# Kernel optimization log

Measured on AMD Instinct MI355X. Metric: run time of the kernel, lower is better.

## Reference

```python
import jax, jax.numpy as jnp
import numpy as np
from jax import lax

SOS_IDX = 1
EOS_IDX = 2

B, T, K = 32, 256, 128


def setup_inputs() -> dict:
    key = jax.random.key(0)
    k1, k2, k3, k4 = jax.random.split(key, 4)
    h = jax.random.normal(k1, (B, T, K), dtype=jnp.float32)
    transition = jax.random.normal(k2, (K, K), dtype=jnp.float32) * 0.1
    y = jax.random.randint(k3, (B, T), 0, K)
    lengths = jnp.maximum(jax.random.randint(k4, (B,), 1, T + 1), 1)
    mask = jnp.arange(T)[None, :] < lengths[:, None]  # [B, T] bool, contiguous prefix
    return {"h": h, "transition": transition, "y": y, "lengths": lengths, "mask": mask}


def reference(h, transition, y, lengths, mask):
    """CRF negative log-likelihood, same math as CRF.nll."""
    b, t_len, k = h.shape
    # crf_scores[b,t,i,j] = h[b,t,j] + transition[i,j]
    scores = h[:, :, None, :] + transition[None, None, :, :]  # [B,T,K,K]

    # Golden path score: score of transition prev_tag -> tag at each valid step.
    prev_y = jnp.concatenate(
        [jnp.full((b, 1), SOS_IDX, dtype=y.dtype), y[:, :-1]], axis=1
    )  # [B,T]
    gold = jnp.take_along_axis(
        jnp.take_along_axis(scores, prev_y[:, :, None, None], axis=2)[:, :, 0, :],
        y[:, :, None],
        axis=2,
    )[:, :, 0]  # [B,T]
    golden_scores = jnp.sum(jnp.where(mask, gold, jnp.zeros((), h.dtype)))

    # Forward (alpha) recurrence in log space; freeze alpha past sequence end.
    alpha0 = scores[:, 0, SOS_IDX, :]  # [B,K] (all lengths >= 1)
    scores_tbkk = jnp.swapaxes(scores, 0, 1)  # [T,B,K,K]
    mask_tb = jnp.swapaxes(mask, 0, 1)  # [T,B]

    def step(alpha, xs):
        s_t, m_t = xs  # [B,K,K], [B]
        new_alpha = jax.nn.logsumexp(s_t + alpha[:, :, None], axis=1)  # [B,K]
        return jnp.where(m_t[:, None], new_alpha, alpha), None

    alpha, _ = lax.scan(step, alpha0, (scores_tbkk[1:], mask_tb[1:]))
    Z = jnp.sum(alpha[:, EOS_IDX])
    loss = (Z - golden_scores) / b
    return loss
```

## Files before the change

### kernel.cpp

```cpp
#include <hip/hip_runtime.h>
#include <stdint.h>

#define SOS_IDX 1
#define EOS_IDX 2
#define Bb 32
#define Tt 256
#define Kk 128
#define SK 136

typedef unsigned short ushort_t;
typedef __attribute__((ext_vector_type(8))) short short8;
typedef __attribute__((ext_vector_type(4))) float float4v;

__device__ __forceinline__ ushort_t f2bf(float x) {
    union { float f; uint32_t u; } c; c.f = x;
    uint32_t u = c.u + 0x7FFFu + ((c.u >> 16) & 1u);
    return (ushort_t)(u >> 16);
}
__device__ __forceinline__ float bf2f(ushort_t s) {
    union { uint32_t u; float f; } c; c.u = ((uint32_t)s) << 16;
    return c.f;
}
__device__ __forceinline__ float bflo(uint32_t u) {
    union { uint32_t u; float f; } c; c.u = u << 16; return c.f;
}
__device__ __forceinline__ float bfhi(uint32_t u) {
    union { uint32_t u; float f; } c; c.u = u & 0xFFFF0000u; return c.f;
}
__device__ __forceinline__ uint32_t pk2bf(float a, float b) {
    union { float f; uint32_t u; } ca, cb; ca.f = a; cb.f = b;
    uint32_t ua = ca.u + 0x7FFFu + ((ca.u >> 16) & 1u);
    uint32_t ub = cb.u + 0x7FFFu + ((cb.u >> 16) & 1u);
    return __builtin_amdgcn_perm(ub, ua, 0x07060302u);
}

__global__ __launch_bounds__(256, 2) void crf_stageA(const float* __restrict__ h,
                                                     const float* __restrict__ trans,
                                                     const int* __restrict__ lengths,
                                                     ushort_t* __restrict__ Qt,
                                                     float* __restrict__ Ls,
                                                     int NC, int CSPAN) {
    const int st = blockIdx.x, c = blockIdx.y, b = blockIdx.z;
    const int tid = threadIdx.x;
    const int lane = tid & 63, w = tid >> 6;
    const int c15 = lane & 15, q = lane >> 4;
    const int len = lengths[b];
    int ts = c * CSPAN; if (ts < 1) ts = 1;
    int te = (c + 1) * CSPAN; if (te > Tt) te = Tt;
    const int tE = te < len ? te : len;
    const size_t qoff = ((size_t)b * NC + c) * (Kk * Kk);
    const int nbase = st * 32;

    if (ts >= tE) {
#pragma unroll
        for (int j = 0; j < 2; ++j) {
            int idx = j * 256 + tid;
            int n = idx & 127, o = idx >> 7;
            uint4 gv; ushort_t* gp = (ushort_t*)&gv;
#pragma unroll
            for (int r = 0; r < 8; ++r) gp[r] = (n == nbase + o * 8 + r) ? (ushort_t)0x3F80 : (ushort_t)0;
            *(uint4*)&Qt[qoff + (size_t)n * Kk + nbase + o * 8] = gv;
        }
        if (tid == 0) Ls[(((size_t)b * NC + c) << 2) + st] = 0.0f;
        return;
    }

    __shared__ __align__(16) ushort_t s_S[2][32 * SK];
    __shared__ float s_wmax[2][4];

    short8 afr[2][4];
#pragma unroll
    for (int round = 0; round < 2; ++round) {
        for (int i = 0; i < 32; ++i) {
            int item = i * 256 + tid;
            int m = item & 63, k = item >> 6;
            s_S[m >> 5][(m & 31) * SK + k] = f2bf(__expf(trans[k * Kk + round * 64 + m]));
        }
        __syncthreads();
        if ((w >> 1) == round) {
            const ushort_t* sb = s_S[w & 1];
#pragma unroll
            for (int mt = 0; mt < 2; ++mt)
#pragma unroll
                for (int kt = 0; kt < 4; ++kt)
                    afr[mt][kt] = *(const short8*)&sb[(mt * 16 + c15) * SK + kt * 32 + q * 8];
        }
        __syncthreads();
    }

#pragma unroll
    for (int j = 0; j < 2; ++j) {
        int idx = j * 256 + tid;
        int nl = idx >> 4, oct = idx & 15;
        short8 z = {0, 0, 0, 0, 0, 0, 0, 0};
        int d = nbase + nl - oct * 8;
        if (d >= 0 && d < 8) z[d] = (short)0x3F80;
        *(short8*)&s_S[0][nl * SK + oct * 8] = z;
    }
    if (tid < 4) s_wmax[0][tid] = 1.0f;

    const float* hb = &h[((size_t)b * Tt) * Kk];
    float4 hp0 = *(const float4*)&hb[(size_t)ts * Kk + w * 32 + q * 4];
    float4 hp1 = *(const float4*)&hb[(size_t)ts * Kk + w * 32 + 16 + q * 4];
    __syncthreads();

    float Lw = 0.0f;
    int cur = 0;
    for (int t = ts; t < tE; ++t) {
        float4 h0 = hp0, h1 = hp1;
        if (t + 1 < tE) {
            hp0 = *(const float4*)&hb[(size_t)(t + 1) * Kk + w * 32 + q * 4];
            hp1 = *(const float4*)&hb[(size_t)(t + 1) * Kk + w * 32 + 16 + q * 4];
        }
        float G = fmaxf(fmaxf(s_wmax[cur][0], s_wmax[cur][1]),
                        fmaxf(s_wmax[cur][2], s_wmax[cur][3]));
        float invG = 1.0f / G;
        Lw += __logf(G);

        float sc0[4], sc1[4];
        sc0[0] = __expf(h0.x) * invG; sc0[1] = __expf(h0.y) * invG;
        sc0[2] = __expf(h0.z) * invG; sc0[3] = __expf(h0.w) * invG;
        sc1[0] = __expf(h1.x) * invG; sc1[1] = __expf(h1.y) * invG;
        sc1[2] = __expf(h1.z) * invG; sc1[3] = __expf(h1.w) * invG;

        short8 bfr[2][4];
        const ushort_t* ps = s_S[cur];
#pragma unroll
        for (int nt = 0; nt < 2; ++nt)
#pragma unroll
            for (int kt = 0; kt < 4; ++kt)
                bfr[nt][kt] = *(const short8*)&ps[(nt * 16 + c15) * SK + kt * 32 + q * 8];

        float4v acc[2][2];
#pragma unroll
        for (int mt = 0; mt < 2; ++mt)
#pragma unroll
            for (int nt = 0; nt < 2; ++nt) acc[mt][nt] = (float4v){0.f, 0.f, 0.f, 0.f};
#pragma unroll
        for (int kt = 0; kt < 4; ++kt)
#pragma unroll
            for (int mt = 0; mt < 2; ++mt)
#pragma unroll
                for (int nt = 0; nt < 2; ++nt)
                    acc[mt][nt] = __builtin_amdgcn_mfma_f32_16x16x32_bf16(
                        afr[mt][kt], bfr[nt][kt], acc[mt][nt], 0, 0, 0);

        int nxt = cur ^ 1;
        ushort_t* pn = s_S[nxt];
        float lmax = 0.0f;
#pragma unroll
        for (int mt = 0; mt < 2; ++mt)
#pragma unroll
            for (int nt = 0; nt < 2; ++nt) {
                float v0 = acc[mt][nt][0] * (mt ? sc1[0] : sc0[0]);
                float v1 = acc[mt][nt][1] * (mt ? sc1[1] : sc0[1]);
                float v2 = acc[mt][nt][2] * (mt ? sc1[2] : sc0[2]);
                float v3 = acc[mt][nt][3] * (mt ? sc1[3] : sc0[3]);
                lmax = fmaxf(lmax, fmaxf(fmaxf(v0, v1), fmaxf(v2, v3)));
                uint2 u; u.x = pk2bf(v0, v1); u.y = pk2bf(v2, v3);
                *(uint2*)&pn[(nt * 16 + c15) * SK + w * 32 + mt * 16 + q * 4] = u;
            }
#pragma unroll
        for (int o = 1; o < 64; o <<= 1) lmax = fmaxf(lmax, __shfl_xor(lmax, o));
        if (lane == 0) s_wmax[nxt][w] = lmax;
        __syncthreads();
        cur = nxt;
    }

    float Gf = fmaxf(fmaxf(s_wmax[cur][0], s_wmax[cur][1]),
                     fmaxf(s_wmax[cur][2], s_wmax[cur][3]));
    float dsc = 1.0f / Gf;
    Lw += __logf(Gf);
    const ushort_t* pc = s_S[cur];
#pragma unroll
    for (int j = 0; j < 2; ++j) {
        int idx = j * 256 + tid;
        int n = idx & 127, o = idx >> 7;
        uint4 gv; ushort_t* gp = (ushort_t*)&gv;
#pragma unroll
        for (int r = 0; r < 8; ++r)
            gp[r] = f2bf(bf2f(pc[(o * 8 + r) * SK + n]) * dsc);
        *(uint4*)&Qt[qoff + (size_t)n * Kk + nbase + o * 8] = gv;
    }
    if (tid == 0) Ls[(((size_t)b * NC + c) << 2) + st] = Lw;
}

__global__ __launch_bounds__(256, 1) void crf_stageB(const float* __restrict__ h,
                                                     const float* __restrict__ trans,
                                                     const int* __restrict__ y,
                                                     const int* __restrict__ lengths,
                                                     const ushort_t* __restrict__ Qt,
                                                     const float* __restrict__ Ls,
                                                     float* __restrict__ out, int NC) {
    const int b = blockIdx.x;
    const int tid = threadIdx.x;
    const int lane = tid & 63, w = tid >> 6;
    const int n = tid >> 1, half = tid & 1;
    const int len = lengths[b];

    __shared__ __align__(16) float vbuf[2][Kk];
    __shared__ float s_wmax[2][4];
    __shared__ float red[4];
    __shared__ float gred[4];

    {
        float g = 0.0f;
        if (tid < len) {
            int yt   = y[b * Tt + tid];
            int prev = (tid == 0) ? SOS_IDX : y[b * Tt + tid - 1];
            g = h[((size_t)b * Tt + tid) * Kk + yt] + trans[prev * Kk + yt];
        }
#pragma unroll
        for (int off = 32; off > 0; off >>= 1) g += __shfl_down(g, off);
        if (lane == 0) gred[w] = g;
    }

    float a0 = h[((size_t)b * Tt) * Kk + n] + trans[SOS_IDX * Kk + n];
    float m0 = a0;
#pragma unroll
    for (int o = 1; o < 64; o <<= 1) m0 = fmaxf(m0, __shfl_xor(m0, o));
    if (lane == 0) red[w] = m0;
    __syncthreads();
    m0 = fmaxf(fmaxf(red[0], red[1]), fmaxf(red[2], red[3]));
    float cacc = m0;
    if (half == 0) vbuf[0][n] = __expf(a0 - m0);
    if (tid < 4) s_wmax[0][tid] = 1.0f;
    if (tid == 0)
        atomicAdd(out, -(gred[0] + gred[1] + gred[2] + gred[3]) * (1.0f / (float)Bb));
    __syncthreads();

    const size_t lbase = (size_t)b * NC;
    uint4 qb[8];
    {
        const uint4* qp = (const uint4*)(Qt + lbase * (Kk * Kk) + n * Kk + half * 64);
#pragma unroll
        for (int r = 0; r < 8; ++r) qb[r] = qp[r];
    }

    int cur = 0;
    for (int ci = 0; ci < NC; ++ci) {
        uint4 qn[8];
        if (ci + 1 < NC) {
            const uint4* qp2 = (const uint4*)(Qt + (lbase + ci + 1) * (Kk * Kk) + n * Kk + half * 64);
#pragma unroll
            for (int r = 0; r < 8; ++r) qn[r] = qp2[r];
        }
        float4 Ls4 = *(const float4*)&Ls[(lbase + ci) << 2];
        float Lref = fmaxf(fmaxf(Ls4.x, Ls4.y), fmaxf(Ls4.z, Ls4.w));
        float eA = __expf((half ? Ls4.z : Ls4.x) - Lref);
        float eB = __expf((half ? Ls4.w : Ls4.y) - Lref);

        float G = fmaxf(fmaxf(s_wmax[cur][0], s_wmax[cur][1]),
                        fmaxf(s_wmax[cur][2], s_wmax[cur][3]));
        float invG = 1.0f / G;
        cacc += __logf(G) + Lref;

        float aA0 = 0.f, aA1 = 0.f, aB0 = 0.f, aB1 = 0.f;
#pragma unroll
        for (int r = 0; r < 8; ++r) {
            uint4 d = qb[r];
            float4 v0 = *(const float4*)&vbuf[cur][half * 64 + r * 8];
            float4 v1 = *(const float4*)&vbuf[cur][half * 64 + r * 8 + 4];
            float* p0 = (r < 4) ? &aA0 : &aB0;
            float* p1 = (r < 4) ? &aA1 : &aB1;
            *p0 = fmaf(bflo(d.x), v0.x, *p0);
            *p1 = fmaf(bfhi(d.x), v0.y, *p1);
            *p0 = fmaf(bflo(d.y), v0.z, *p0);
            *p1 = fmaf(bfhi(d.y), v0.w, *p1);
            *p0 = fmaf(bflo(d.z), v1.x, *p0);
            *p1 = fmaf(bfhi(d.z), v1.y, *p1);
            *p0 = fmaf(bflo(d.w), v1.z, *p0);
            *p1 = fmaf(bfhi(d.w), v1.w, *p1);
        }
        float s = (fmaf(eA, aA0 + aA1, eB * (aB0 + aB1))) * invG;
        s += __shfl_xor(s, 1);

        float wm = s;
#pragma unroll
        for (int o = 1; o < 64; o <<= 1) wm = fmaxf(wm, __shfl_xor(wm, o));
        int nxt = cur ^ 1;
        if (half == 0) vbuf[nxt][n] = s;
        if (lane == 0) s_wmax[nxt][w] = wm;
        __syncthreads();
        cur = nxt;
        if (ci + 1 < NC) {
#pragma unroll
            for (int r = 0; r < 8; ++r) qb[r] = qn[r];
        }
    }

    if (tid == 0) {
        atomicAdd(out, (cacc + __logf(vbuf[cur][EOS_IDX])) * (1.0f / (float)Bb));
    }
}

extern "C" void kernel_launch(void* const* d_in, const int* in_sizes, int n_in,
                              void* d_out, int out_size, void* d_ws, size_t ws_size,
                              hipStream_t stream) {
    const float* h       = (const float*)d_in[0];
    const float* trans   = (const float*)d_in[1];
    const int*   y       = (const int*)d_in[2];
    const int*   lengths = (const int*)d_in[3];
    float* out = (float*)d_out;

    int NC = 8;
    while (NC > 1) {
        size_t need = (size_t)Bb * NC * Kk * Kk * 2 + (size_t)Bb * NC * 16;
        if (need <= ws_size) break;
        NC >>= 1;
    }
    int CSPAN = Tt / NC;
    ushort_t* Qt = (ushort_t*)d_ws;
    float* Ls = (float*)((char*)d_ws + (size_t)Bb * NC * Kk * Kk * 2);

    hipMemsetAsync(out, 0, sizeof(float), stream);
    crf_stageA<<<dim3(4, NC, Bb), 256, 0, stream>>>(h, trans, lengths, Qt, Ls, NC, CSPAN);
    crf_stageB<<<Bb, 256, 0, stream>>>(h, trans, y, lengths, Qt, Ls, out, NC);
}
```

Measured before the change: 136.7 us.

## Increase chunk count, precompute exp(h) in LDS, renormalize every four steps, widen stageB

Stage A now loads and exponentiates the chunk's emissions into shared memory as bf16 up front, and skips fully masked chunks instead of writing identity matrices. It also performs the max-reduction and renormalization only every fourth step instead of every step. The number of time chunks doubles from 8 to 16, giving more parallelism in stage A and shorter serial chains. Stage B uses 512 threads with four lanes per output row, iterates only over chunks that hold valid steps, and applies the same sparse renormalization. The risks are overflow or precision loss in bf16 from delayed rescaling, and a larger workspace requirement that must fit in ws_size, since NC can no longer fall below 8.

```diff
diff --git a/kernel.cpp b/kernel.cpp
--- a/kernel.cpp
+++ b/kernel.cpp
@@ -48,25 +48,20 @@
     int ts = c * CSPAN; if (ts < 1) ts = 1;
     int te = (c + 1) * CSPAN; if (te > Tt) te = Tt;
     const int tE = te < len ? te : len;
+    if (ts >= tE) return;
+    const int nsteps = tE - ts;
     const size_t qoff = ((size_t)b * NC + c) * (Kk * Kk);
     const int nbase = st * 32;
 
-    if (ts >= tE) {
-#pragma unroll
-        for (int j = 0; j < 2; ++j) {
-            int idx = j * 256 + tid;
-            int n = idx & 127, o = idx >> 7;
-            uint4 gv; ushort_t* gp = (ushort_t*)&gv;
-#pragma unroll
-            for (int r = 0; r < 8; ++r) gp[r] = (n == nbase + o * 8 + r) ? (ushort_t)0x3F80 : (ushort_t)0;
-            *(uint4*)&Qt[qoff + (size_t)n * Kk + nbase + o * 8] = gv;
-        }
-        if (tid == 0) Ls[(((size_t)b * NC + c) << 2) + st] = 0.0f;
-        return;
-    }
-
     __shared__ __align__(16) ushort_t s_S[2][32 * SK];
+    __shared__ __align__(16) ushort_t s_ehb[32][Kk];
     __shared__ float s_wmax[2][4];
+
+    for (int tl = w; tl < nsteps; tl += 4) {
+        const float* hr = &h[((size_t)b * Tt + ts + tl) * Kk];
+        s_ehb[tl][lane]      = f2bf(__expf(hr[lane]));
+        s_ehb[tl][lane + 64] = f2bf(__expf(hr[lane + 64]));
+    }
 
     short8 afr[2][4];
 #pragma unroll
@@ -97,31 +92,30 @@
         if (d >= 0 && d < 8) z[d] = (short)0x3F80;
         *(short8*)&s_S[0][nl * SK + oct * 8] = z;
     }
-    if (tid < 4) s_wmax[0][tid] = 1.0f;
-
-    const float* hb = &h[((size_t)b * Tt) * Kk];
-    float4 hp0 = *(const float4*)&hb[(size_t)ts * Kk + w * 32 + q * 4];
-    float4 hp1 = *(const float4*)&hb[(size_t)ts * Kk + w * 32 + 16 + q * 4];
     __syncthreads();
 
-    float Lw = 0.0f;
+    float L = 0.0f;
     int cur = 0;
-    for (int t = ts; t < tE; ++t) {
-        float4 h0 = hp0, h1 = hp1;
-        if (t + 1 < tE) {
-            hp0 = *(const float4*)&hb[(size_t)(t + 1) * Kk + w * 32 + q * 4];
-            hp1 = *(const float4*)&hb[(size_t)(t + 1) * Kk + w * 32 + 16 + q * 4];
-        }
-        float G = fmaxf(fmaxf(s_wmax[cur][0], s_wmax[cur][1]),
-                        fmaxf(s_wmax[cur][2], s_wmax[cur][3]));
-        float invG = 1.0f / G;
-        Lw += __logf(G);
+    for (int s = 0; s < nsteps; ++s) {
+        float invG = 1.0f;
+        if (s > 0 && (s & 3) == 0) {
+            int ms = ((s >> 2) - 1) & 1;
+            float g = fmaxf(fmaxf(s_wmax[ms][0], s_wmax[ms][1]),
+                            fmaxf(s_wmax[ms][2], s_wmax[ms][3]));
+            invG = 1.0f / g;
+            L += __logf(g);
+        }
+        const bool isMark = ((s & 3) == 3) || (s == nsteps - 1);
 
         float sc0[4], sc1[4];
-        sc0[0] = __expf(h0.x) * invG; sc0[1] = __expf(h0.y) * invG;
-        sc0[2] = __expf(h0.z) * invG; sc0[3] = __expf(h0.w) * invG;
-        sc1[0] = __expf(h1.x) * invG; sc1[1] = __expf(h1.y) * invG;
-        sc1[2] = __expf(h1.z) * invG; sc1[3] = __expf(h1.w) * invG;
+        {
+            uint2 u0 = *(const uint2*)&s_ehb[s][w * 32 + q * 4];
+            uint2 u1 = *(const uint2*)&s_ehb[s][w * 32 + 16 + q * 4];
+            sc0[0] = bflo(u0.x) * invG; sc0[1] = bfhi(u0.x) * invG;
+            sc0[2] = bflo(u0.y) * invG; sc0[3] = bfhi(u0.y) * invG;
+            sc1[0] = bflo(u1.x) * invG; sc1[1] = bfhi(u1.x) * invG;
+            sc1[2] = bflo(u1.y) * invG; sc1[3] = bfhi(u1.y) * invG;
+        }
 
         short8 bfr[2][4];
         const ushort_t* ps = s_S[cur];
@@ -160,17 +154,20 @@
                 uint2 u; u.x = pk2bf(v0, v1); u.y = pk2bf(v2, v3);
                 *(uint2*)&pn[(nt * 16 + c15) * SK + w * 32 + mt * 16 + q * 4] = u;
             }
-#pragma unroll
-        for (int o = 1; o < 64; o <<= 1) lmax = fmaxf(lmax, __shfl_xor(lmax, o));
-        if (lane == 0) s_wmax[nxt][w] = lmax;
+        if (isMark) {
+#pragma unroll
+            for (int o = 1; o < 64; o <<= 1) lmax = fmaxf(lmax, __shfl_xor(lmax, o));
+            if (lane == 0) s_wmax[(s >> 2) & 1][w] = lmax;
+        }
         __syncthreads();
         cur = nxt;
     }
 
-    float Gf = fmaxf(fmaxf(s_wmax[cur][0], s_wmax[cur][1]),
-                     fmaxf(s_wmax[cur][2], s_wmax[cur][3]));
+    int fs = ((nsteps - 1) >> 2) & 1;
+    float Gf = fmaxf(fmaxf(s_wmax[fs][0], s_wmax[fs][1]),
+                     fmaxf(s_wmax[fs][2], s_wmax[fs][3]));
     float dsc = 1.0f / Gf;
-    Lw += __logf(Gf);
+    L += __logf(Gf);
     const ushort_t* pc = s_S[cur];
 #pragma unroll
     for (int j = 0; j < 2; ++j) {
@@ -182,28 +179,29 @@
             gp[r] = f2bf(bf2f(pc[(o * 8 + r) * SK + n]) * dsc);
         *(uint4*)&Qt[qoff + (size_t)n * Kk + nbase + o * 8] = gv;
     }
-    if (tid == 0) Ls[(((size_t)b * NC + c) << 2) + st] = Lw;
-}
-
-__global__ __launch_bounds__(256, 1) void crf_stageB(const float* __restrict__ h,
+    if (tid == 0) Ls[(((size_t)b * NC + c) << 2) + st] = L;
+}
+
+__global__ __launch_bounds__(512, 1) void crf_stageB(const float* __restrict__ h,
                                                      const float* __restrict__ trans,
                                                      const int* __restrict__ y,
                                                      const int* __restrict__ lengths,
                                                      const ushort_t* __restrict__ Qt,
                                                      const float* __restrict__ Ls,
-                                                     float* __restrict__ out, int NC) {
+                                                     float* __restrict__ out,
+                                                     int NC, int CSPAN) {
     const int b = blockIdx.x;
     const int tid = threadIdx.x;
     const int lane = tid & 63, w = tid >> 6;
-    const int n = tid >> 1, half = tid & 1;
+    const int n = tid >> 2, qr = tid & 3;
     const int len = lengths[b];
 
     __shared__ __align__(16) float vbuf[2][Kk];
-    __shared__ float s_wmax[2][4];
-    __shared__ float red[4];
+    __shared__ float s_wmax[2][8];
+    __shared__ float red[8];
     __shared__ float gred[4];
 
-    {
+    if (w < 4) {
         float g = 0.0f;
         if (tid < len) {
             int yt   = y[b * Tt + tid];
@@ -221,71 +219,84 @@
     for (int o = 1; o < 64; o <<= 1) m0 = fmaxf(m0, __shfl_xor(m0, o));
     if (lane == 0) red[w] = m0;
     __syncthreads();
-    m0 = fmaxf(fmaxf(red[0], red[1]), fmaxf(red[2], red[3]));
+    {
+        float4 r0 = *(const float4*)&red[0];
+        float4 r1 = *(const float4*)&red[4];
+        m0 = fmaxf(fmaxf(fmaxf(r0.x, r0.y), fmaxf(r0.z, r0.w)),
+                   fmaxf(fmaxf(r1.x, r1.y), fmaxf(r1.z, r1.w)));
+    }
     float cacc = m0;
-    if (half == 0) vbuf[0][n] = __expf(a0 - m0);
-    if (tid < 4) s_wmax[0][tid] = 1.0f;
+    if (qr == 0) vbuf[0][n] = __expf(a0 - m0);
+
+    const int NCR = (len <= 1) ? 0 : min(NC, (len + CSPAN - 1) / CSPAN);
+    const size_t lbase = (size_t)b * NC;
+    uint4 qb[4];
+    if (NCR > 0) {
+        const uint4* qp = (const uint4*)(Qt + lbase * (Kk * Kk) + n * Kk + qr * 32);
+#pragma unroll
+        for (int r = 0; r < 4; ++r) qb[r] = qp[r];
+    }
+    __syncthreads();
     if (tid == 0)
         atomicAdd(out, -(gred[0] + gred[1] + gred[2] + gred[3]) * (1.0f / (float)Bb));
-    __syncthreads();
-
-    const size_t lbase = (size_t)b * NC;
-    uint4 qb[8];
-    {
-        const uint4* qp = (const uint4*)(Qt + lbase * (Kk * Kk) + n * Kk + half * 64);
-#pragma unroll
-        for (int r = 0; r < 8; ++r) qb[r] = qp[r];
-    }
 
     int cur = 0;
-    for (int ci = 0; ci < NC; ++ci) {
-        uint4 qn[8];
-        if (ci + 1 < NC) {
-            const uint4* qp2 = (const uint4*)(Qt + (lbase + ci + 1) * (Kk * Kk) + n * Kk + half * 64);
-#pragma unroll
-            for (int r = 0; r < 8; ++r) qn[r] = qp2[r];
+    for (int ci = 0; ci < NCR; ++ci) {
+        uint4 qn[4];
+        if (ci + 1 < NCR) {
+            const uint4* qp2 = (const uint4*)(Qt + (lbase + ci + 1) * (Kk * Kk) + n * Kk + qr * 32);
+#pragma unroll
+            for (int r = 0; r < 4; ++r) qn[r] = qp2[r];
         }
         float4 Ls4 = *(const float4*)&Ls[(lbase + ci) << 2];
         float Lref = fmaxf(fmaxf(Ls4.x, Ls4.y), fmaxf(Ls4.z, Ls4.w));
-        float eA = __expf((half ? Ls4.z : Ls4.x) - Lref);
-        float eB = __expf((half ? Ls4.w : Ls4.y) - Lref);
-
-        float G = fmaxf(fmaxf(s_wmax[cur][0], s_wmax[cur][1]),
-                        fmaxf(s_wmax[cur][2], s_wmax[cur][3]));
-        float invG = 1.0f / G;
-        cacc += __logf(G) + Lref;
-
-        float aA0 = 0.f, aA1 = 0.f, aB0 = 0.f, aB1 = 0.f;
-#pragma unroll
-        for (int r = 0; r < 8; ++r) {
+        float lsq = (qr == 0) ? Ls4.x : (qr == 1) ? Ls4.y : (qr == 2) ? Ls4.z : Ls4.w;
+        float eQ = __expf(lsq - Lref);
+        float invG = 1.0f;
+        if (ci > 0 && (ci & 3) == 0) {
+            int ms = ((ci >> 2) - 1) & 1;
+            float4 r0 = *(const float4*)&s_wmax[ms][0];
+            float4 r1 = *(const float4*)&s_wmax[ms][4];
+            float g = fmaxf(fmaxf(fmaxf(r0.x, r0.y), fmaxf(r0.z, r0.w)),
+                            fmaxf(fmaxf(r1.x, r1.y), fmaxf(r1.z, r1.w)));
+            invG = 1.0f / g;
+            cacc += __logf(g);
+        }
+        cacc += Lref;
+
+        float acc0 = 0.0f, acc1 = 0.0f;
+#pragma unroll
+        for (int r = 0; r < 4; ++r) {
             uint4 d = qb[r];
-            float4 v0 = *(const float4*)&vbuf[cur][half * 64 + r * 8];
-            float4 v1 = *(const float4*)&vbuf[cur][half * 64 + r * 8 + 4];
-            float* p0 = (r < 4) ? &aA0 : &aB0;
-            float* p1 = (r < 4) ? &aA1 : &aB1;
-            *p0 = fmaf(bflo(d.x), v0.x, *p0);
-            *p1 = fmaf(bfhi(d.x), v0.y, *p1);
-            *p0 = fmaf(bflo(d.y), v0.z, *p0);
-            *p1 = fmaf(bfhi(d.y), v0.w, *p1);
-            *p0 = fmaf(bflo(d.z), v1.x, *p0);
-            *p1 = fmaf(bfhi(d.z), v1.y, *p1);
-            *p0 = fmaf(bflo(d.w), v1.z, *p0);
-            *p1 = fmaf(bfhi(d.w), v1.w, *p1);
-        }
-        float s = (fmaf(eA, aA0 + aA1, eB * (aB0 + aB1))) * invG;
+            float4 v0 = *(const float4*)&vbuf[cur][qr * 32 + r * 8];
+            float4 v1 = *(const float4*)&vbuf[cur][qr * 32 + r * 8 + 4];
+            acc0 = fmaf(bflo(d.x), v0.x, acc0);
+            acc1 = fmaf(bfhi(d.x), v0.y, acc1);
+            acc0 = fmaf(bflo(d.y), v0.z, acc0);
+            acc1 = fmaf(bfhi(d.y), v0.w, acc1);
+            acc0 = fmaf(bflo(d.z), v1.x, acc0);
+            acc1 = fmaf(bfhi(d.z), v1.y, acc1);
+            acc0 = fmaf(bflo(d.w), v1.z, acc0);
+            acc1 = fmaf(bfhi(d.w), v1.w, acc1);
+        }
+        float s = (acc0 + acc1) * (eQ * invG);
         s += __shfl_xor(s, 1);
-
-        float wm = s;
-#pragma unroll
-        for (int o = 1; o < 64; o <<= 1) wm = fmaxf(wm, __shfl_xor(wm, o));
+        s += __shfl_xor(s, 2);
+
+        const bool isMark = ((ci & 3) == 3) || (ci == NCR - 1);
+        if (isMark) {
+            float wm = s;
+#pragma unroll
+            for (int o = 1; o < 64; o <<= 1) wm = fmaxf(wm, __shfl_xor(wm, o));
+            if (lane == 0) s_wmax[(ci >> 2) & 1][w] = wm;
+        }
         int nxt = cur ^ 1;
-        if (half == 0) vbuf[nxt][n] = s;
-        if (lane == 0) s_wmax[nxt][w] = wm;
+        if (qr == 0) vbuf[nxt][n] = s;
         __syncthreads();
         cur = nxt;
-        if (ci + 1 < NC) {
-#pragma unroll
-            for (int r = 0; r < 8; ++r) qb[r] = qn[r];
+        if (ci + 1 < NCR) {
+#pragma unroll
+            for (int r = 0; r < 4; ++r) qb[r] = qn[r];
         }
     }
 
@@ -303,8 +314,8 @@
     const int*   lengths = (const int*)d_in[3];
     float* out = (float*)d_out;
 
-    int NC = 8;
-    while (NC > 1) {
+    int NC = 16;
+    while (NC > 8) {
         size_t need = (size_t)Bb * NC * Kk * Kk * 2 + (size_t)Bb * NC * 16;
         if (need <= ws_size) break;
         NC >>= 1;
@@ -315,5 +326,5 @@
 
     hipMemsetAsync(out, 0, sizeof(float), stream);
     crf_stageA<<<dim3(4, NC, Bb), 256, 0, stream>>>(h, trans, lengths, Qt, Ls, NC, CSPAN);
-    crf_stageB<<<Bb, 256, 0, stream>>>(h, trans, y, lengths, Qt, Ls, out, NC);
-}
+    crf_stageB<<<Bb, 512, 0, stream>>>(h, trans, y, lengths, Qt, Ls, out, NC, CSPAN);
+}
```

Measured after the change: 115.0 us. 15.9% less time.
